# Kernel optimization log

Hardware: AMD Instinct MI355X
Metric: run time of the kernel (lower is better)

The kernel has to match this reference:

```python
import jax, jax.numpy as jnp
import numpy as np

NEG_SLOPE = 0.2

def _smlp(x, w, b):
    # torch nn.Linear convention: y = x @ w.T + b, then leaky_relu(0.2)
    return jax.nn.leaky_relu(x @ w.T + b, NEG_SLOPE)

_gather = jax.vmap(lambda a, i: a[i])  # (N,C),(N,k) -> (N,k,C), vmapped over batch

def _lfa(points, feats, idx, w, b):
    # points: (B,N,3), feats: (B,N,F_D), idx: (B,N,k)
    knn_p = _gather(points, idx)                      # (B,N,k,3)
    rel = points[:, :, None, :] - knn_p               # (B,N,k,3)
    dist = jnp.linalg.norm(rel, axis=-1, keepdims=True)
    geo = jnp.concatenate([rel, dist], axis=-1)       # (B,N,k,4)
    mlp = _smlp(geo, w, b)                            # (B,N,k,d)
    knn_f = _gather(feats, idx)                       # (B,N,k,F_D)
    return jnp.concatenate([mlp, knn_f], axis=-1).mean(axis=2)  # (B,N,d+F_D)

def setup_inputs() -> dict:
    key = jax.random.key(0)
    ks = jax.random.split(key, 12)
    B, N, K, D = 2, 65536, 32, 64
    pts = jax.random.normal(ks[0], (B, N, 3), jnp.float32)
    feats = jax.random.normal(ks[1], (B, N, D), jnp.float32)
    idx = jax.random.randint(ks[2], (B, N, K), 0, N)
    def lin(k, o, i):
        bound = 1.0 / np.sqrt(i)
        kw, kb = jax.random.split(k)
        return (jax.random.uniform(kw, (o, i), jnp.float32, -bound, bound),
                jax.random.uniform(kb, (o,), jnp.float32, -bound, bound))
    w_init, b_init = lin(ks[3], D // 4, D)
    w_lfa1, b_lfa1 = lin(ks[4], D // 4, 4)
    w_lfa2, b_lfa2 = lin(ks[5], D // 2, 4)
    w_final, b_final = lin(ks[6], D, D)
    w_res, b_res = lin(ks[7], D, D)
    return {"points": pts, "features": feats, "knn_indices": idx,
            "w_init": w_init, "b_init": b_init,
            "w_lfa1": w_lfa1, "b_lfa1": b_lfa1,
            "w_lfa2": w_lfa2, "b_lfa2": b_lfa2,
            "w_final": w_final, "b_final": b_final,
            "w_res": w_res, "b_res": b_res}

def reference(points, features, knn_indices, w_init, b_init,
              w_lfa1, b_lfa1, w_lfa2, b_lfa2,
              w_final, b_final, w_res, b_res):
    x = _smlp(features, w_init, b_init)               # (B,N,16)
    x = _lfa(points, x, knn_indices, w_lfa1, b_lfa1)  # (B,N,32)
    x = _lfa(points, x, knn_indices, w_lfa2, b_lfa2)  # (B,N,64)
    x = _smlp(x, w_final, b_final)                    # (B,N,64)
    residual = _smlp(features, w_res, b_res)          # (B,N,64)
    return x + residual
```

## Files before the change

kernel.cpp:

```cpp
#include <hip/hip_runtime.h>
#include <math.h>

#define NPTS 65536

typedef unsigned short ushort_t;
typedef unsigned int uint_t;
typedef __attribute__((ext_vector_type(8))) short bf16x8;
typedef __attribute__((ext_vector_type(4))) float f32x4;

__device__ __forceinline__ float lrelu(float x) {
  return fmaf(0.4f, fabsf(x), 0.6f * x);
}
__device__ __forceinline__ ushort_t f2b(float f) {
  union { float f; uint_t u; } v; v.f = f;
  uint_t u = v.u + (0x7fffu + ((v.u >> 16) & 1u));
  return (ushort_t)(u >> 16);
}
__device__ __forceinline__ float b2f_lo(uint_t u) {
  union { uint_t u; float f; } v; v.u = u << 16; return v.f;
}
__device__ __forceinline__ float b2f_hi(uint_t u) {
  union { uint_t u; float f; } v; v.u = u & 0xffff0000u; return v.f;
}
__device__ __forceinline__ bf16x8 cvt8(const float* p) {
  float4 a = ((const float4*)p)[0];
  float4 b = ((const float4*)p)[1];
  float f[8] = {a.x, a.y, a.z, a.w, b.x, b.y, b.z, b.w};
  bf16x8 r;
#pragma unroll
  for (int j = 0; j < 8; ++j) r[j] = (short)f2b(f[j]);
  return r;
}

__device__ __forceinline__ int block_pbase() {
  int bid = blockIdx.x;
  if (gridDim.x == 2048) {
    int g = bid >> 3, x = bid & 7;
    return (x >> 2) * NPTS + (g * 4 + (x & 3)) * 64;
  }
  return bid * 64;
}

__global__ __launch_bounds__(256) void k_init(
    const float* __restrict__ feats, const float* __restrict__ w,
    const float* __restrict__ bia, ushort_t* __restrict__ x1,
    const float* __restrict__ pts, float4* __restrict__ pts4,
    const float* __restrict__ wf, const float* __restrict__ wr,
    ushort_t* __restrict__ wfb, ushort_t* __restrict__ wrb, int BN) {
  __shared__ float wt[64 * 16];
  int t = threadIdx.x;
  if (blockIdx.x < 2) {
    const float* src = blockIdx.x ? wr : wf;
    ushort_t* dst = blockIdx.x ? wrb : wfb;
    for (int e = t; e < 4096; e += 256) dst[e] = f2b(src[e]);
  }
  for (int e = t; e < 1024; e += 256) {
    int o = e >> 6, i = e & 63;
    wt[i * 16 + o] = w[e];
  }
  __syncthreads();
  int p = blockIdx.x * 256 + t;
  if (p >= BN) return;
  const float* pp = pts + (size_t)p * 3;
  pts4[p] = make_float4(pp[0], pp[1], pp[2], 0.0f);
  float acc[16];
#pragma unroll
  for (int o = 0; o < 16; ++o) acc[o] = bia[o];
  const float* xr = feats + (size_t)p * 64;
#pragma unroll 8
  for (int i = 0; i < 64; ++i) {
    float xi = xr[i];
    const float4* w4 = (const float4*)&wt[i * 16];
#pragma unroll
    for (int q = 0; q < 4; ++q) {
      float4 wv = w4[q];
      acc[q * 4 + 0] = fmaf(xi, wv.x, acc[q * 4 + 0]);
      acc[q * 4 + 1] = fmaf(xi, wv.y, acc[q * 4 + 1]);
      acc[q * 4 + 2] = fmaf(xi, wv.z, acc[q * 4 + 2]);
      acc[q * 4 + 3] = fmaf(xi, wv.w, acc[q * 4 + 3]);
    }
  }
  union { ushort_t u[16]; uint4 v[2]; } pk;
#pragma unroll
  for (int o = 0; o < 16; ++o) pk.u[o] = f2b(lrelu(acc[o]));
  uint4* op = (uint4*)(x1 + (size_t)p * 16);
  op[0] = pk.v[0];
  op[1] = pk.v[1];
}

__global__ __launch_bounds__(256) void k_lfa1(
    const float4* __restrict__ pts4, const ushort_t* __restrict__ fin,
    const int* __restrict__ idx, const float* __restrict__ w,
    const float* __restrict__ bia, ushort_t* __restrict__ out, int BN) {
  int t = threadIdx.x;
  int p = block_pbase() + (t >> 2);
  int sub = t & 3;
  if (p >= BN) return;
  int base = p & ~(NPTS - 1);
  float4 mp = pts4[p];
  float4 wreg[4];
  float breg[4];
  const float4* wrow = (const float4*)w + sub * 4;
#pragma unroll
  for (int o = 0; o < 4; ++o) { wreg[o] = wrow[o]; breg[o] = bia[sub * 4 + o]; }
  float macc[4] = {0.f, 0.f, 0.f, 0.f};
  float facc[4] = {0.f, 0.f, 0.f, 0.f};
  const int4* iv4 = (const int4*)(idx + (size_t)p * 32);
#pragma unroll 2
  for (int kk = 0; kk < 8; ++kk) {
    int4 iv = iv4[kk];
    int js[4] = {iv.x, iv.y, iv.z, iv.w};
#pragma unroll
    for (int u = 0; u < 4; ++u) {
      int j = base + js[u];
      float4 pj = pts4[j];
      float rx = mp.x - pj.x, ry = mp.y - pj.y, rz = mp.z - pj.z;
      float d = sqrtf(fmaf(rx, rx, fmaf(ry, ry, rz * rz)));
#pragma unroll
      for (int o = 0; o < 4; ++o) {
        float4 wv = wreg[o];
        float s = fmaf(rx, wv.x, fmaf(ry, wv.y, fmaf(rz, wv.z, fmaf(d, wv.w, breg[o]))));
        macc[o] += lrelu(s);
      }
      uint2 fv = *((const uint2*)(fin + (size_t)j * 16) + sub);
      facc[0] += b2f_lo(fv.x); facc[1] += b2f_hi(fv.x);
      facc[2] += b2f_lo(fv.y); facc[3] += b2f_hi(fv.y);
    }
  }
  const float inv = 1.0f / 32.0f;
  ushort_t* orow = out + (size_t)p * 32;
  union { ushort_t u[4]; uint2 v; } pm, pf;
#pragma unroll
  for (int q = 0; q < 4; ++q) {
    pm.u[q] = f2b(macc[q] * inv);
    pf.u[q] = f2b(facc[q] * inv);
  }
  ((uint2*)orow)[sub] = pm.v;
  ((uint2*)orow)[4 + sub] = pf.v;
}

__global__ __launch_bounds__(256) void k_lfa2f(
    const float4* __restrict__ pts4, const ushort_t* __restrict__ fin,
    const int* __restrict__ idx, const float* __restrict__ w,
    const float* __restrict__ bia, const float* __restrict__ feats,
    const ushort_t* __restrict__ wfb, const float* __restrict__ bfi,
    const ushort_t* __restrict__ wrb, const float* __restrict__ bri,
    float* __restrict__ out, int BN) {
  int t = threadIdx.x;
  int lane = t & 63, wave = t >> 6;
  int n = lane & 15, quad = lane >> 4;
  int wbase = block_pbase() + wave * 16;
  int p0 = wbase + n;
  int p = p0 < BN ? p0 : BN - 1;
  int base = p & ~(NPTS - 1);
  int sub = quad;
  float4 mp = pts4[p];
  float4 wreg[8];
  float breg[8];
  const float4* wrow = (const float4*)w + sub * 8;
#pragma unroll
  for (int o = 0; o < 8; ++o) { wreg[o] = wrow[o]; breg[o] = bia[sub * 8 + o]; }
  float macc[8], facc[8];
#pragma unroll
  for (int o = 0; o < 8; ++o) { macc[o] = 0.f; facc[o] = 0.f; }
  const int4* iv4 = (const int4*)(idx + (size_t)p * 32);
#pragma unroll 2
  for (int kk = 0; kk < 8; ++kk) {
    int4 iv = iv4[kk];
    int js[4] = {iv.x, iv.y, iv.z, iv.w};
#pragma unroll
    for (int u = 0; u < 4; ++u) {
      int j = base + js[u];
      float4 pj = pts4[j];
      float rx = mp.x - pj.x, ry = mp.y - pj.y, rz = mp.z - pj.z;
      float d = sqrtf(fmaf(rx, rx, fmaf(ry, ry, rz * rz)));
#pragma unroll
      for (int o = 0; o < 8; ++o) {
        float4 wv = wreg[o];
        float s = fmaf(rx, wv.x, fmaf(ry, wv.y, fmaf(rz, wv.z, fmaf(d, wv.w, breg[o]))));
        macc[o] += lrelu(s);
      }
      uint4 fv = *((const uint4*)(fin + (size_t)j * 32) + sub);
      facc[0] += b2f_lo(fv.x); facc[1] += b2f_hi(fv.x);
      facc[2] += b2f_lo(fv.y); facc[3] += b2f_hi(fv.y);
      facc[4] += b2f_lo(fv.z); facc[5] += b2f_hi(fv.z);
      facc[6] += b2f_lo(fv.w); facc[7] += b2f_hi(fv.w);
    }
  }
  const float inv = 1.0f / 32.0f;
  bf16x8 Ax0, Ax1;
#pragma unroll
  for (int o = 0; o < 8; ++o) {
    Ax0[o] = (short)f2b(macc[o] * inv);
    Ax1[o] = (short)f2b(facc[o] * inv);
  }
  const float* af = feats + (size_t)p * 64 + quad * 8;
  bf16x8 Af0 = cvt8(af), Af1 = cvt8(af + 32);
  float y[16];
#pragma unroll
  for (int nt = 0; nt < 4; ++nt) {
    f32x4 acc = {0.f, 0.f, 0.f, 0.f};
    int woff = (nt * 16 + n) * 64 + quad * 8;
    bf16x8 Bf0 = *((const bf16x8*)(wfb + woff));
    bf16x8 Bf1 = *((const bf16x8*)(wfb + woff + 32));
    acc = __builtin_amdgcn_mfma_f32_16x16x32_bf16(Ax0, Bf0, acc, 0, 0, 0);
    acc = __builtin_amdgcn_mfma_f32_16x16x32_bf16(Ax1, Bf1, acc, 0, 0, 0);
    float bv = bfi[nt * 16 + n];
#pragma unroll
    for (int r = 0; r < 4; ++r) y[nt * 4 + r] = lrelu(acc[r] + bv);
  }
#pragma unroll
  for (int nt = 0; nt < 4; ++nt) {
    f32x4 acc = {0.f, 0.f, 0.f, 0.f};
    int woff = (nt * 16 + n) * 64 + quad * 8;
    bf16x8 Br0 = *((const bf16x8*)(wrb + woff));
    bf16x8 Br1 = *((const bf16x8*)(wrb + woff + 32));
    acc = __builtin_amdgcn_mfma_f32_16x16x32_bf16(Af0, Br0, acc, 0, 0, 0);
    acc = __builtin_amdgcn_mfma_f32_16x16x32_bf16(Af1, Br1, acc, 0, 0, 0);
    float bv = bri[nt * 16 + n];
#pragma unroll
    for (int r = 0; r < 4; ++r) {
      int row = wbase + quad * 4 + r;
      if (row < BN) out[(size_t)row * 64 + nt * 16 + n] = y[nt * 4 + r] + lrelu(acc[r] + bv);
    }
  }
}

extern "C" void kernel_launch(void* const* d_in, const int* in_sizes, int n_in,
                              void* d_out, int out_size, void* d_ws, size_t ws_size,
                              hipStream_t stream) {
  const float* pts    = (const float*)d_in[0];
  const float* feats  = (const float*)d_in[1];
  const int*   idx    = (const int*)d_in[2];
  const float* w_init = (const float*)d_in[3];
  const float* b_init = (const float*)d_in[4];
  const float* w_l1   = (const float*)d_in[5];
  const float* b_l1   = (const float*)d_in[6];
  const float* w_l2   = (const float*)d_in[7];
  const float* b_l2   = (const float*)d_in[8];
  const float* w_f    = (const float*)d_in[9];
  const float* b_f    = (const float*)d_in[10];
  const float* w_r    = (const float*)d_in[11];
  const float* b_r    = (const float*)d_in[12];
  float* out = (float*)d_out;

  int BN = in_sizes[2] / 32;
  ushort_t* x1 = (ushort_t*)d_ws;
  ushort_t* x2 = x1 + (size_t)BN * 16;
  float4* pts4 = (float4*)(x2 + (size_t)BN * 32);
  ushort_t* wfb = (ushort_t*)(pts4 + BN);
  ushort_t* wrb = wfb + 4096;

  int blocks_pt = (BN + 255) / 256;
  int blocks_g = (BN + 63) / 64;

  k_init<<<blocks_pt, 256, 0, stream>>>(feats, w_init, b_init, x1, pts, pts4,
                                        w_f, w_r, wfb, wrb, BN);
  k_lfa1<<<blocks_g, 256, 0, stream>>>(pts4, x1, idx, w_l1, b_l1, x2, BN);
  k_lfa2f<<<blocks_g, 256, 0, stream>>>(pts4, x2, idx, w_l2, b_l2, feats,
                                        wfb, b_f, wrb, b_r, out, BN);
}
```

Measured before the change: 271.2 us.

## Compute both LFA geometric MLPs in first gather pass, skip second point gather

The second LFA's geometric MLP depends only on points and neighbor indices, so it is now computed in the first LFA kernel alongside the first MLP and written out as a bf16 buffer. The second kernel no longer gathers neighbor points or evaluates the geometric MLP. It only gathers the features and reads the precomputed geometry term, with a deeper unroll. This removes a full random gather of point coordinates and the associated ALU work, at the cost of an extra 32-channel intermediate write and read and more register pressure in the first kernel.

```diff
diff --git a/kernel.cpp b/kernel.cpp
--- a/kernel.cpp
+++ b/kernel.cpp
@@ -88,23 +88,33 @@
   op[1] = pk.v[1];
 }
 
-__global__ __launch_bounds__(256) void k_lfa1(
+__global__ __launch_bounds__(256) void k_lfa1g(
     const float4* __restrict__ pts4, const ushort_t* __restrict__ fin,
-    const int* __restrict__ idx, const float* __restrict__ w,
-    const float* __restrict__ bia, ushort_t* __restrict__ out, int BN) {
+    const int* __restrict__ idx, const float* __restrict__ w1,
+    const float* __restrict__ b1, const float* __restrict__ w2,
+    const float* __restrict__ b2, ushort_t* __restrict__ x2out,
+    ushort_t* __restrict__ g2out, int BN) {
   int t = threadIdx.x;
   int p = block_pbase() + (t >> 2);
   int sub = t & 3;
   if (p >= BN) return;
   int base = p & ~(NPTS - 1);
   float4 mp = pts4[p];
-  float4 wreg[4];
-  float breg[4];
-  const float4* wrow = (const float4*)w + sub * 4;
-#pragma unroll
-  for (int o = 0; o < 4; ++o) { wreg[o] = wrow[o]; breg[o] = bia[sub * 4 + o]; }
-  float macc[4] = {0.f, 0.f, 0.f, 0.f};
-  float facc[4] = {0.f, 0.f, 0.f, 0.f};
+  float4 w1r[4];
+  float b1r[4];
+  const float4* wrow1 = (const float4*)w1 + sub * 4;
+#pragma unroll
+  for (int o = 0; o < 4; ++o) { w1r[o] = wrow1[o]; b1r[o] = b1[sub * 4 + o]; }
+  float4 w2r[8];
+  float b2r[8];
+  const float4* wrow2 = (const float4*)w2 + sub * 8;
+#pragma unroll
+  for (int o = 0; o < 8; ++o) { w2r[o] = wrow2[o]; b2r[o] = b2[sub * 8 + o]; }
+  float macc1[4] = {0.f, 0.f, 0.f, 0.f};
+  float facc1[4] = {0.f, 0.f, 0.f, 0.f};
+  float macc2[8];
+#pragma unroll
+  for (int o = 0; o < 8; ++o) macc2[o] = 0.f;
   const int4* iv4 = (const int4*)(idx + (size_t)p * 32);
 #pragma unroll 2
   for (int kk = 0; kk < 8; ++kk) {
@@ -114,35 +124,44 @@
     for (int u = 0; u < 4; ++u) {
       int j = base + js[u];
       float4 pj = pts4[j];
+      uint2 fv = *((const uint2*)(fin + (size_t)j * 16) + sub);
       float rx = mp.x - pj.x, ry = mp.y - pj.y, rz = mp.z - pj.z;
       float d = sqrtf(fmaf(rx, rx, fmaf(ry, ry, rz * rz)));
 #pragma unroll
       for (int o = 0; o < 4; ++o) {
-        float4 wv = wreg[o];
-        float s = fmaf(rx, wv.x, fmaf(ry, wv.y, fmaf(rz, wv.z, fmaf(d, wv.w, breg[o]))));
-        macc[o] += lrelu(s);
+        float4 wv = w1r[o];
+        float s = fmaf(rx, wv.x, fmaf(ry, wv.y, fmaf(rz, wv.z, fmaf(d, wv.w, b1r[o]))));
+        macc1[o] += lrelu(s);
       }
-      uint2 fv = *((const uint2*)(fin + (size_t)j * 16) + sub);
-      facc[0] += b2f_lo(fv.x); facc[1] += b2f_hi(fv.x);
-      facc[2] += b2f_lo(fv.y); facc[3] += b2f_hi(fv.y);
+#pragma unroll
+      for (int o = 0; o < 8; ++o) {
+        float4 wv = w2r[o];
+        float s = fmaf(rx, wv.x, fmaf(ry, wv.y, fmaf(rz, wv.z, fmaf(d, wv.w, b2r[o]))));
+        macc2[o] += lrelu(s);
+      }
+      facc1[0] += b2f_lo(fv.x); facc1[1] += b2f_hi(fv.x);
+      facc1[2] += b2f_lo(fv.y); facc1[3] += b2f_hi(fv.y);
     }
   }
   const float inv = 1.0f / 32.0f;
-  ushort_t* orow = out + (size_t)p * 32;
+  ushort_t* orow = x2out + (size_t)p * 32;
   union { ushort_t u[4]; uint2 v; } pm, pf;
 #pragma unroll
   for (int q = 0; q < 4; ++q) {
-    pm.u[q] = f2b(macc[q] * inv);
-    pf.u[q] = f2b(facc[q] * inv);
+    pm.u[q] = f2b(macc1[q] * inv);
+    pf.u[q] = f2b(facc1[q] * inv);
   }
   ((uint2*)orow)[sub] = pm.v;
   ((uint2*)orow)[4 + sub] = pf.v;
+  union { ushort_t u[8]; uint4 v; } pg;
+#pragma unroll
+  for (int q = 0; q < 8; ++q) pg.u[q] = f2b(macc2[q] * inv);
+  ((uint4*)(g2out + (size_t)p * 32))[sub] = pg.v;
 }
 
 __global__ __launch_bounds__(256) void k_lfa2f(
-    const float4* __restrict__ pts4, const ushort_t* __restrict__ fin,
-    const int* __restrict__ idx, const float* __restrict__ w,
-    const float* __restrict__ bia, const float* __restrict__ feats,
+    const ushort_t* __restrict__ fin, const int* __restrict__ idx,
+    const ushort_t* __restrict__ g2, const float* __restrict__ feats,
     const ushort_t* __restrict__ wfb, const float* __restrict__ bfi,
     const ushort_t* __restrict__ wrb, const float* __restrict__ bri,
     float* __restrict__ out, int BN) {
@@ -153,34 +172,18 @@
   int p0 = wbase + n;
   int p = p0 < BN ? p0 : BN - 1;
   int base = p & ~(NPTS - 1);
-  int sub = quad;
-  float4 mp = pts4[p];
-  float4 wreg[8];
-  float breg[8];
-  const float4* wrow = (const float4*)w + sub * 8;
-#pragma unroll
-  for (int o = 0; o < 8; ++o) { wreg[o] = wrow[o]; breg[o] = bia[sub * 8 + o]; }
-  float macc[8], facc[8];
-#pragma unroll
-  for (int o = 0; o < 8; ++o) { macc[o] = 0.f; facc[o] = 0.f; }
+  float facc[8];
+#pragma unroll
+  for (int o = 0; o < 8; ++o) facc[o] = 0.f;
   const int4* iv4 = (const int4*)(idx + (size_t)p * 32);
-#pragma unroll 2
+#pragma unroll 4
   for (int kk = 0; kk < 8; ++kk) {
     int4 iv = iv4[kk];
     int js[4] = {iv.x, iv.y, iv.z, iv.w};
 #pragma unroll
     for (int u = 0; u < 4; ++u) {
       int j = base + js[u];
-      float4 pj = pts4[j];
-      float rx = mp.x - pj.x, ry = mp.y - pj.y, rz = mp.z - pj.z;
-      float d = sqrtf(fmaf(rx, rx, fmaf(ry, ry, rz * rz)));
-#pragma unroll
-      for (int o = 0; o < 8; ++o) {
-        float4 wv = wreg[o];
-        float s = fmaf(rx, wv.x, fmaf(ry, wv.y, fmaf(rz, wv.z, fmaf(d, wv.w, breg[o]))));
-        macc[o] += lrelu(s);
-      }
-      uint4 fv = *((const uint4*)(fin + (size_t)j * 32) + sub);
+      uint4 fv = *((const uint4*)(fin + (size_t)j * 32) + quad);
       facc[0] += b2f_lo(fv.x); facc[1] += b2f_hi(fv.x);
       facc[2] += b2f_lo(fv.y); facc[3] += b2f_hi(fv.y);
       facc[4] += b2f_lo(fv.z); facc[5] += b2f_hi(fv.z);
@@ -188,12 +191,10 @@
     }
   }
   const float inv = 1.0f / 32.0f;
-  bf16x8 Ax0, Ax1;
-#pragma unroll
-  for (int o = 0; o < 8; ++o) {
-    Ax0[o] = (short)f2b(macc[o] * inv);
-    Ax1[o] = (short)f2b(facc[o] * inv);
-  }
+  bf16x8 Ax0 = *((const bf16x8*)(g2 + (size_t)p * 32 + quad * 8));
+  bf16x8 Ax1;
+#pragma unroll
+  for (int o = 0; o < 8; ++o) Ax1[o] = (short)f2b(facc[o] * inv);
   const float* af = feats + (size_t)p * 64 + quad * 8;
   bf16x8 Af0 = cvt8(af), Af1 = cvt8(af + 32);
   float y[16];
@@ -250,13 +251,15 @@
   float4* pts4 = (float4*)(x2 + (size_t)BN * 32);
   ushort_t* wfb = (ushort_t*)(pts4 + BN);
   ushort_t* wrb = wfb + 4096;
+  ushort_t* g2 = wrb + 4096;
 
   int blocks_pt = (BN + 255) / 256;
   int blocks_g = (BN + 63) / 64;
 
   k_init<<<blocks_pt, 256, 0, stream>>>(feats, w_init, b_init, x1, pts, pts4,
                                         w_f, w_r, wfb, wrb, BN);
-  k_lfa1<<<blocks_g, 256, 0, stream>>>(pts4, x1, idx, w_l1, b_l1, x2, BN);
-  k_lfa2f<<<blocks_g, 256, 0, stream>>>(pts4, x2, idx, w_l2, b_l2, feats,
-                                        wfb, b_f, wrb, b_r, out, BN);
-}
+  k_lfa1g<<<blocks_g, 256, 0, stream>>>(pts4, x1, idx, w_l1, b_l1, w_l2, b_l2,
+                                        x2, g2, BN);
+  k_lfa2f<<<blocks_g, 256, 0, stream>>>(x2, idx, g2, feats, wfb, b_f, wrb, b_r,
+                                        out, BN);
+}
```

After: 256.3 us. -5.5%, faster.
